# Performance work log

Measured on AMD Instinct MI355X. Metric: run time of the kernel, lower is better.

Reference implementation:

```python
import jax, jax.numpy as jnp
import numpy as np

N, E, IN_DIM, H, D, EDGE_DIM, T = 50000, 800000, 128, 4, 32, 32, 8
NEG_SLOPE = 0.2


def setup_inputs() -> dict:
    key = jax.random.key(0)
    ks = jax.random.split(key, 12)
    s = 0.1  # xavier-ish scale
    return {
        "h": jax.random.normal(ks[0], (N, IN_DIM), jnp.float32),
        "W": jax.random.normal(ks[1], (IN_DIM, D * H), jnp.float32) * s,
        "edge_emb": jax.random.normal(ks[2], (T, EDGE_DIM), jnp.float32) * s,
        "W_r": jax.random.normal(ks[3], (T, EDGE_DIM, EDGE_DIM * H), jnp.float32) * s,
        "a_l": jax.random.normal(ks[4], (1, H, D), jnp.float32) * s,
        "a_r": jax.random.normal(ks[5], (1, H, D), jnp.float32) * s,
        "a_e": jax.random.normal(ks[6], (1, H, EDGE_DIM), jnp.float32) * s,
        "res_w": jax.random.normal(ks[7], (IN_DIM, D * H), jnp.float32) * s,
        "res_b": jnp.zeros((D * H,), jnp.float32),
        "row": jax.random.randint(ks[8], (E,), 0, N),  # src node per edge
        "col": jax.random.randint(ks[9], (E,), 0, N),  # dst node per edge
        "etype": jax.random.randint(ks[10], (E,), 0, T),
    }


def reference(h, W, edge_emb, W_r, a_l, a_r, a_e, res_w, res_b, row, col, etype):
    # node projection: [N, H, D]
    emb = (h @ W).reshape(-1, H, D)

    # TypedLinear on edge-type embeddings. Since edge features depend only on
    # etype, compute the per-type result once, then gather per edge.
    e_t = jnp.einsum('te,tef->tf', edge_emb, W_r).reshape(T, H, EDGE_DIM)
    h_e_t = (a_e * e_t).sum(-1)            # [T, H]

    h_l = (a_l * emb).sum(-1)              # [N, H]
    h_r = (a_r * emb).sum(-1)              # [N, H]
    scores = h_l[row] + h_r[col] + h_e_t[etype]          # [E, H]
    scores = jax.nn.leaky_relu(scores, NEG_SLOPE)

    # segment softmax over edges sharing the same destination node (col)
    m = jax.ops.segment_max(scores, col, num_segments=N)  # [N, H]
    ex = jnp.exp(scores - m[col])
    denom = jax.ops.segment_sum(ex, col, num_segments=N)
    alpha = ex / denom[col]                # [E, H]

    # u_mul_e + scatter-sum to destination nodes
    msg = emb[row] * alpha[:, :, None]     # [E, H, D]
    agg = jax.ops.segment_sum(msg, col, num_segments=N)   # [N, H, D]

    # original permutes to [N, D, H] before flattening (d-major layout)
    out = jnp.transpose(agg, (0, 2, 1)).reshape(-1, D * H)
    out = out + h @ res_w + res_b          # residual
    return jax.nn.elu(out)
```

## Files before the change

kernel.cpp:

```cpp
#include <hip/hip_runtime.h>
#include <math.h>

#define NH 4
#define EDIM 32
#define NEG_SLOPE 0.2f
#define BSH 5
#define BCAP 1024

typedef __attribute__((ext_vector_type(8))) short short8;
typedef __attribute__((ext_vector_type(4))) float f32x4;
typedef __attribute__((ext_vector_type(2))) float f32x2;

__device__ __forceinline__ unsigned short f2bf(float f) {
    unsigned int x = __builtin_bit_cast(unsigned int, f);
    unsigned int r = (x + 0x7fffu + ((x >> 16) & 1u)) >> 16;
    return (unsigned short)r;
}
__device__ __forceinline__ float bf2f(unsigned short u) {
    unsigned int x = ((unsigned int)u) << 16;
    return __builtin_bit_cast(float, x);
}

__global__ __launch_bounds__(256) void k_prep(
    const float* __restrict__ W, const float* __restrict__ Rw,
    unsigned short* __restrict__ Wt, unsigned short* __restrict__ Rwt,
    int* __restrict__ bucket_cursor,
    const float* __restrict__ edge_emb, const float* __restrict__ W_r,
    const float* __restrict__ a_e, float* __restrict__ h_e_t)
{
    int tid = threadIdx.x;
    if (blockIdx.x < 64) {
        int idx = blockIdx.x * 256 + tid;
        int n = idx >> 7, k = idx & 127;
        Wt[n * 128 + k]  = f2bf(W[k * 128 + n]);
        Rwt[n * 128 + k] = f2bf(Rw[k * 128 + n]);
        if (idx < 2048) bucket_cursor[idx] = idx * BCAP;
    } else {
        int j = blockIdx.x - 64;
        int t = j >> 2;
        int ec = (j & 3) * 2 + (tid >> 7);
        int rem = tid & 127;
        float v = 0.f;
#pragma unroll
        for (int u = 0; u < 4; ++u) {
            int e = ec * 4 + u;
            v += edge_emb[t * EDIM + e] * W_r[(size_t)(t * EDIM + e) * 128 + rem];
        }
        v *= a_e[rem];
#pragma unroll
        for (int off = 16; off >= 1; off >>= 1)
            v += __shfl_xor(v, off);
        if ((rem & 31) == 0) atomicAdd(&h_e_t[t * NH + (rem >> 5)], v);
    }
}

__global__ __launch_bounds__(256) void k_gemm_fill(
    const float* __restrict__ A, const unsigned short* __restrict__ Wt,
    const unsigned short* __restrict__ Rwt, const float* __restrict__ Rb,
    const float* __restrict__ a_l, const float* __restrict__ a_r,
    unsigned short* __restrict__ EmbBf, unsigned short* __restrict__ ResBf,
    float* __restrict__ h_l, float* __restrict__ h_r, int M,
    const int* __restrict__ row, const int* __restrict__ col,
    const int* __restrict__ etype, int* __restrict__ bucket_cursor,
    unsigned* __restrict__ ebuf, int E, int NB, int nFill)
{
    __shared__ char lds[49152];
    int tid = threadIdx.x;

    if ((int)blockIdx.x < nFill) {
        int* bins = (int*)lds;
        int* base = bins + 2048;
        for (int i = tid; i < NB; i += 256) bins[i] = 0;
        __syncthreads();
        int lo = blockIdx.x * 4096;
        int ccol[16];
#pragma unroll
        for (int u = 0; u < 16; ++u) {
            int i = lo + tid + u * 256;
            int c = (i < E) ? col[i] : -1;
            ccol[u] = c;
            if (c >= 0) atomicAdd(&bins[c >> BSH], 1);
        }
        __syncthreads();
        for (int i = tid; i < NB; i += 256) {
            int c = bins[i];
            base[i] = c ? atomicAdd(&bucket_cursor[i], c) : 0;
            bins[i] = 0;
        }
        __syncthreads();
#pragma unroll
        for (int u = 0; u < 16; ++u) {
            int i = lo + tid + u * 256;
            int c = ccol[u];
            if (c >= 0) {
                int bk = c >> BSH;
                int p = base[bk] + atomicAdd(&bins[bk], 1);
                ebuf[p] = (unsigned)row[i] | ((unsigned)etype[i] << 16)
                        | ((unsigned)(c & 31) << 24);
            }
        }
        return;
    }

    int m0 = ((int)blockIdx.x - nFill) * 64;
#pragma unroll
    for (int i = 0; i < 4; ++i) {
        int c = tid + 256 * i;
        int r = c >> 4, kc = c & 15;
        int grow = m0 + r;
        float4 v0 = make_float4(0.f, 0.f, 0.f, 0.f), v1 = v0;
        if (grow < M) {
            v0 = *(const float4*)&A[(size_t)grow * 128 + kc * 8];
            v1 = *(const float4*)&A[(size_t)grow * 128 + kc * 8 + 4];
        }
        union { unsigned short u[8]; uint4 v; } p;
        p.u[0] = f2bf(v0.x); p.u[1] = f2bf(v0.y); p.u[2] = f2bf(v0.z); p.u[3] = f2bf(v0.w);
        p.u[4] = f2bf(v1.x); p.u[5] = f2bf(v1.y); p.u[6] = f2bf(v1.z); p.u[7] = f2bf(v1.w);
        int b = (r * 256 + kc * 16) ^ ((r & 7) << 4);
        *(uint4*)&lds[b] = p.v;
    }
#pragma unroll
    for (int i = 0; i < 8; ++i) {
        int c = tid + 256 * i;
        int n = c >> 4, kc = c & 15;
        uint4 v = *(const uint4*)&Wt[n * 128 + kc * 8];
        int b = 16384 + ((n * 256 + kc * 16) ^ ((n & 7) << 4));
        *(uint4*)&lds[b] = v;
    }
    __syncthreads();

    int w = tid >> 6, lane = tid & 63;
    int g = lane >> 4, l15 = lane & 15;
    int lrow = w * 16 + l15;

    short8 a[4];
#pragma unroll
    for (int s = 0; s < 4; ++s)
        a[s] = *(const short8*)&lds[(lrow * 256 + s * 64 + g * 16) ^ ((lrow & 7) << 4)];

    f32x4 acc[8];
#pragma unroll
    for (int f = 0; f < 8; ++f) acc[f] = (f32x4){0.f, 0.f, 0.f, 0.f};

#pragma unroll
    for (int f = 0; f < 8; ++f) {
        int n = f * 16 + l15;
        int nsw = (n & 7) << 4;
#pragma unroll
        for (int s = 0; s < 4; ++s) {
            short8 b = *(const short8*)&lds[16384 + ((n * 256 + s * 64 + g * 16) ^ nsw)];
            acc[f] = __builtin_amdgcn_mfma_f32_16x16x32_bf16(a[s], b, acc[f], 0, 0, 0);
        }
    }
#pragma unroll
    for (int f = 0; f < 8; ++f) {
        int col2 = f * 16 + l15;
#pragma unroll
        for (int reg = 0; reg < 4; ++reg) {
            int grow = m0 + w * 16 + g * 4 + reg;
            if (grow < M) EmbBf[(size_t)grow * 128 + col2] = f2bf(acc[f][reg]);
        }
    }
    {
        float alv[8], arv[8];
#pragma unroll
        for (int f = 0; f < 8; ++f) {
            alv[f] = a_l[f * 16 + l15];
            arv[f] = a_r[f * 16 + l15];
        }
#pragma unroll
        for (int reg = 0; reg < 4; ++reg) {
            float4 hl4, hr4;
#pragma unroll
            for (int hh = 0; hh < 4; ++hh) {
                float pl = alv[2 * hh] * acc[2 * hh][reg] + alv[2 * hh + 1] * acc[2 * hh + 1][reg];
                float pr = arv[2 * hh] * acc[2 * hh][reg] + arv[2 * hh + 1] * acc[2 * hh + 1][reg];
#pragma unroll
                for (int off = 8; off >= 1; off >>= 1) {
                    pl += __shfl_xor(pl, off);
                    pr += __shfl_xor(pr, off);
                }
                (&hl4.x)[hh] = pl;
                (&hr4.x)[hh] = pr;
            }
            int grow = m0 + w * 16 + g * 4 + reg;
            if (l15 == 0 && grow < M) {
                *(float4*)&h_l[(size_t)grow * 4] = hl4;
                *(float4*)&h_r[(size_t)grow * 4] = hr4;
            }
        }
    }

    __syncthreads();
#pragma unroll
    for (int i = 0; i < 8; ++i) {
        int c = tid + 256 * i;
        int n = c >> 4, kc = c & 15;
        uint4 v = *(const uint4*)&Rwt[n * 128 + kc * 8];
        int b = 16384 + ((n * 256 + kc * 16) ^ ((n & 7) << 4));
        *(uint4*)&lds[b] = v;
    }
    __syncthreads();

#pragma unroll
    for (int f = 0; f < 8; ++f) acc[f] = (f32x4){0.f, 0.f, 0.f, 0.f};
#pragma unroll
    for (int f = 0; f < 8; ++f) {
        int n = f * 16 + l15;
        int nsw = (n & 7) << 4;
#pragma unroll
        for (int s = 0; s < 4; ++s) {
            short8 b = *(const short8*)&lds[16384 + ((n * 256 + s * 64 + g * 16) ^ nsw)];
            acc[f] = __builtin_amdgcn_mfma_f32_16x16x32_bf16(a[s], b, acc[f], 0, 0, 0);
        }
    }
#pragma unroll
    for (int f = 0; f < 8; ++f) {
        int col2 = f * 16 + l15;
        float bias = Rb[col2];
#pragma unroll
        for (int reg = 0; reg < 4; ++reg) {
            int grow = m0 + w * 16 + g * 4 + reg;
            if (grow < M) ResBf[(size_t)grow * 128 + col2] = f2bf(acc[f][reg] + bias);
        }
    }
}

__global__ __launch_bounds__(256) void k_sort_aggregate(
    const unsigned* __restrict__ ebuf, const int* __restrict__ bucket_cursor,
    const float* __restrict__ h_l, const float* __restrict__ h_e_t,
    const float* __restrict__ h_r, const unsigned short* __restrict__ embBf,
    const unsigned short* __restrict__ resBf, float* __restrict__ out, int N)
{
    __shared__ int sedge[BCAP];
    __shared__ int cnt[32];
    __shared__ int scn[33];
    __shared__ char shalpha[4 * 1536];

    int b = blockIdx.x;
    int tid = threadIdx.x;
    int seg = b * BCAP;
    int m = bucket_cursor[b] - seg;

    if (tid < 32) cnt[tid] = 0;
    __syncthreads();
    for (int i = tid; i < m; i += 256)
        atomicAdd(&cnt[(ebuf[seg + i] >> 24) & 31], 1);
    __syncthreads();
    if (tid < 32) {
        int v = cnt[tid];
        int s = v;
#pragma unroll
        for (int off = 1; off < 32; off <<= 1) {
            int u2 = __shfl_up(s, off);
            if (tid >= off) s += u2;
        }
        scn[tid + 1] = s;
        if (tid == 0) scn[0] = 0;
        cnt[tid] = s - v;
    }
    __syncthreads();
    for (int i = tid; i < m; i += 256) {
        unsigned e = ebuf[seg + i];
        int p = atomicAdd(&cnt[(e >> 24) & 31], 1);
        sedge[p] = (int)(e & 0x00FFFFFFu);
    }
    __syncthreads();

    int w = tid >> 6, lane = tid & 63;
    int myh = lane >> 4;
    int l31 = lane & 31;
    int hq = l31 >> 3;
    int sel = lane >> 5;
    char* wb = &shalpha[w * 1536];
    const char* ab2 = wb + 256 + hq * 260;
    const char* embByte = (const char*)embBf;

    for (int it = 0; it < 8; ++it) {
        int nd = it * 4 + w;
        int n = b * 32 + nd;
        if (n >= N) break;
        int st0 = scn[nd];
        int deg = scn[nd + 1] - st0;
        float4 hrv = *(const float4*)&h_r[(size_t)n * 4];

        if (deg <= 64) {
            bool act = lane < deg;
            float p0 = 0.f, p1 = 0.f, p2 = 0.f, p3 = 0.f;
            if (act) {
                int pk = sedge[st0 + lane];
                int r = pk & 0xffff;
                float4 hl = *(const float4*)&h_l[(size_t)r * 4];
                float4 he = *(const float4*)&h_e_t[(size_t)(pk >> 16) * 4];
                float sc0 = hl.x + he.x + hrv.x; sc0 = sc0 > 0.f ? sc0 : NEG_SLOPE * sc0;
                float sc1 = hl.y + he.y + hrv.y; sc1 = sc1 > 0.f ? sc1 : NEG_SLOPE * sc1;
                float sc2 = hl.z + he.z + hrv.z; sc2 = sc2 > 0.f ? sc2 : NEG_SLOPE * sc2;
                float sc3 = hl.w + he.w + hrv.w; sc3 = sc3 > 0.f ? sc3 : NEG_SLOPE * sc3;
                p0 = __expf(sc0); p1 = __expf(sc1);
                p2 = __expf(sc2); p3 = __expf(sc3);
                *(int*)(wb + lane * 4) = (pk & 0xffff) << 8;
                *(float*)(wb + 256 + 0 * 260 + lane * 4) = p0;
                *(float*)(wb + 256 + 1 * 260 + lane * 4) = p1;
                *(float*)(wb + 256 + 2 * 260 + lane * 4) = p2;
                *(float*)(wb + 256 + 3 * 260 + lane * 4) = p3;
            }
            float d0 = p0, d1 = p1, d2 = p2, d3 = p3;
#pragma unroll
            for (int off = 32; off >= 1; off >>= 1) {
                d0 += __shfl_xor(d0, off); d1 += __shfl_xor(d1, off);
                d2 += __shfl_xor(d2, off); d3 += __shfl_xor(d3, off);
            }
            float den = hq == 0 ? d0 : hq == 1 ? d1 : hq == 2 ? d2 : d3;
            float inv = (deg > 0) ? __builtin_amdgcn_rcpf(den) : 0.f;

            f32x4 acc4 = (f32x4){0.f, 0.f, 0.f, 0.f};
            for (int q = 0; q < deg; q += 8) {
                unsigned ro[4]; float aq[4];
#pragma unroll
                for (int u = 0; u < 4; ++u) {
                    int qe = q + 2 * u + sel;
                    int qc = qe < deg ? qe : deg - 1;
                    ro[u] = *(const unsigned*)(wb + qc * 4);
                    float av = *(const float*)(ab2 + qc * 4);
                    aq[u] = (qe < deg) ? av : 0.f;
                }
                uint2 ev[4];
#pragma unroll
                for (int u = 0; u < 4; ++u)
                    ev[u] = *(const uint2*)(embByte + (size_t)(ro[u] + l31 * 8));
#pragma unroll
                for (int u = 0; u < 4; ++u) {
                    f32x4 ef;
                    ef.x = __builtin_bit_cast(float, ev[u].x << 16);
                    ef.y = __builtin_bit_cast(float, ev[u].x & 0xffff0000u);
                    ef.z = __builtin_bit_cast(float, ev[u].y << 16);
                    ef.w = __builtin_bit_cast(float, ev[u].y & 0xffff0000u);
                    acc4 = __builtin_elementwise_fma(
                        ef, (f32x4){aq[u], aq[u], aq[u], aq[u]}, acc4);
                }
            }
            acc4.x += __shfl_xor(acc4.x, 32);
            acc4.y += __shfl_xor(acc4.y, 32);
            acc4.z += __shfl_xor(acc4.z, 32);
            acc4.w += __shfl_xor(acc4.w, 32);

            if (lane < 32) {
                size_t ob = (size_t)n * 128;
                int bj = lane * 4;
                int h0 = bj >> 5;
#pragma unroll
                for (int u = 0; u < 4; ++u) {
                    int d = (bj + u) & 31;
                    float o = acc4[u] * inv + bf2f(resBf[ob + d * 4 + h0]);
                    out[ob + d * 4 + h0] = o > 0.f ? o : expm1f(o);
                }
            }
        } else {
            f32x2 acc2 = (f32x2){0.f, 0.f};
            float d0 = 0.f, d1 = 0.f, d2 = 0.f, d3 = 0.f;
            for (int base2 = 0; base2 < deg; base2 += 64) {
                int el = base2 + lane;
                if (el < deg) {
                    int pk = sedge[st0 + el];
                    float4 hl = *(const float4*)&h_l[(size_t)(pk & 0xffff) * 4];
                    float4 he = *(const float4*)&h_e_t[(size_t)(pk >> 16) * 4];
                    float sc0 = hl.x + he.x + hrv.x; sc0 = sc0 > 0.f ? sc0 : NEG_SLOPE * sc0;
                    float sc1 = hl.y + he.y + hrv.y; sc1 = sc1 > 0.f ? sc1 : NEG_SLOPE * sc1;
                    float sc2 = hl.z + he.z + hrv.z; sc2 = sc2 > 0.f ? sc2 : NEG_SLOPE * sc2;
                    float sc3 = hl.w + he.w + hrv.w; sc3 = sc3 > 0.f ? sc3 : NEG_SLOPE * sc3;
                    d0 += __expf(sc0); d1 += __expf(sc1);
                    d2 += __expf(sc2); d3 += __expf(sc3);
                }
            }
#pragma unroll
            for (int off = 32; off >= 1; off >>= 1) {
                d0 += __shfl_xor(d0, off); d1 += __shfl_xor(d1, off);
                d2 += __shfl_xor(d2, off); d3 += __shfl_xor(d3, off);
            }
            float den = myh == 0 ? d0 : myh == 1 ? d1 : myh == 2 ? d2 : d3;
            float inv = __builtin_amdgcn_rcpf(den);
            for (int base2 = 0; base2 < deg; base2 += 64) {
                int el = base2 + lane;
                float p0 = 0.f, p1 = 0.f, p2 = 0.f, p3 = 0.f;
                int r = 0;
                if (el < deg) {
                    int pk = sedge[st0 + el];
                    r = pk & 0xffff;
                    float4 hl = *(const float4*)&h_l[(size_t)r * 4];
                    float4 he = *(const float4*)&h_e_t[(size_t)(pk >> 16) * 4];
                    float sc0 = hl.x + he.x + hrv.x; sc0 = sc0 > 0.f ? sc0 : NEG_SLOPE * sc0;
                    float sc1 = hl.y + he.y + hrv.y; sc1 = sc1 > 0.f ? sc1 : NEG_SLOPE * sc1;
                    float sc2 = hl.z + he.z + hrv.z; sc2 = sc2 > 0.f ? sc2 : NEG_SLOPE * sc2;
                    float sc3 = hl.w + he.w + hrv.w; sc3 = sc3 > 0.f ? sc3 : NEG_SLOPE * sc3;
                    p0 = __expf(sc0); p1 = __expf(sc1);
                    p2 = __expf(sc2); p3 = __expf(sc3);
                }
                int cmax = (deg - base2 < 64) ? (deg - base2) : 64;
                for (int qq = 0; qq < cmax; ++qq) {
                    int rq = __shfl(r, qq);
                    float a0 = __shfl(p0, qq), a1 = __shfl(p1, qq);
                    float a2 = __shfl(p2, qq), a3 = __shfl(p3, qq);
                    float aqv = myh == 0 ? a0 : myh == 1 ? a1 : myh == 2 ? a2 : a3;
                    unsigned int ev = *(const unsigned int*)&embBf[(size_t)rq * 128 + lane * 2];
                    f32x2 ef;
                    ef.x = __builtin_bit_cast(float, ev << 16);
                    ef.y = __builtin_bit_cast(float, ev & 0xffff0000u);
                    acc2 = __builtin_elementwise_fma(ef, (f32x2){aqv, aqv}, acc2);
                }
            }
            int j0 = lane * 2;
            int h0 = j0 >> 5, dd0 = j0 & 31;
            size_t ob = (size_t)n * 128;
            float o0 = acc2.x * inv + bf2f(resBf[ob + dd0 * 4 + h0]);
            float o1 = acc2.y * inv + bf2f(resBf[ob + (dd0 + 1) * 4 + h0]);
            out[ob + dd0 * 4 + h0] = o0 > 0.f ? o0 : expm1f(o0);
            out[ob + (dd0 + 1) * 4 + h0] = o1 > 0.f ? o1 : expm1f(o1);
        }
    }
}

extern "C" void kernel_launch(void* const* d_in, const int* in_sizes, int n_in,
                              void* d_out, int out_size, void* d_ws, size_t ws_size,
                              hipStream_t stream)
{
    const float* h        = (const float*)d_in[0];
    const float* W        = (const float*)d_in[1];
    const float* edge_emb = (const float*)d_in[2];
    const float* W_r      = (const float*)d_in[3];
    const float* a_l      = (const float*)d_in[4];
    const float* a_r      = (const float*)d_in[5];
    const float* a_e      = (const float*)d_in[6];
    const float* res_w    = (const float*)d_in[7];
    const float* res_b    = (const float*)d_in[8];
    const int*   row      = (const int*)d_in[9];
    const int*   col      = (const int*)d_in[10];
    const int*   etype    = (const int*)d_in[11];
    float* out = (float*)d_out;

    int N = in_sizes[0] / 128;
    int E = in_sizes[9];
    int T = in_sizes[2] / EDIM;
    int NB = (N + 31) >> BSH;

    char* ws = (char*)d_ws;
    size_t off = 0;
    auto alloc = [&](size_t bytes) -> char* {
        char* p = ws + off;
        off = (off + bytes + 255) & ~(size_t)255;
        return p;
    };
    unsigned short* embBf = (unsigned short*)alloc((size_t)N * 128 * 2);
    unsigned short* resBf = (unsigned short*)alloc((size_t)N * 128 * 2);
    unsigned short* Wt    = (unsigned short*)alloc((size_t)128 * 128 * 2);
    unsigned short* Rwt   = (unsigned short*)alloc((size_t)128 * 128 * 2);
    float* h_l   = (float*)alloc((size_t)N * 4 * 4);
    float* h_r   = (float*)alloc((size_t)N * 4 * 4);
    float* h_e_t = (float*)alloc((size_t)T * 4 * 4);
    int* bucket_cursor = (int*)alloc(2048 * 4);
    unsigned* ebuf = (unsigned*)alloc((size_t)(NB + 1) * BCAP * 4);

    int nFill = (E + 4095) / 4096;
    int nGemm = (N + 63) / 64;

    hipMemsetAsync(h_e_t, 0, (size_t)T * NH * 4, stream);
    hipLaunchKernelGGL(k_prep, dim3(64 + T * 4), dim3(256), 0, stream,
                       W, res_w, Wt, Rwt, bucket_cursor,
                       edge_emb, W_r, a_e, h_e_t);
    hipLaunchKernelGGL(k_gemm_fill, dim3(nFill + nGemm), dim3(256), 0, stream,
                       h, Wt, Rwt, res_b, a_l, a_r, embBf, resBf, h_l, h_r, N,
                       row, col, etype, bucket_cursor, ebuf, E, NB, nFill);
    hipLaunchKernelGGL(k_sort_aggregate, dim3(NB), dim3(256), 0, stream,
                       ebuf, bucket_cursor, h_l, h_e_t, h_r, embBf, resBf, out, N);
}
```

Measured before the change: 94.22 us.

## Move edge bucketing fill into prep kernel and split GEMM into its own launch

Result: slower. 99.00 us (+5.1%).

```diff
diff --git a/kernel.cpp b/kernel.cpp
--- a/kernel.cpp
+++ b/kernel.cpp
@@ -21,22 +21,29 @@
     return __builtin_bit_cast(float, x);
 }
 
-__global__ __launch_bounds__(256) void k_prep(
+__global__ __launch_bounds__(256) void k_prep_fill(
     const float* __restrict__ W, const float* __restrict__ Rw,
     unsigned short* __restrict__ Wt, unsigned short* __restrict__ Rwt,
-    int* __restrict__ bucket_cursor,
     const float* __restrict__ edge_emb, const float* __restrict__ W_r,
-    const float* __restrict__ a_e, float* __restrict__ h_e_t)
+    const float* __restrict__ a_e, float* __restrict__ h_e_t,
+    const int* __restrict__ row, const int* __restrict__ col,
+    const int* __restrict__ etype, int* __restrict__ bucket_cursor,
+    unsigned* __restrict__ ebuf, int E, int NB, int T)
 {
+    __shared__ int bins[2048];
+    __shared__ int base[2048];
     int tid = threadIdx.x;
-    if (blockIdx.x < 64) {
-        int idx = blockIdx.x * 256 + tid;
+    int bid = blockIdx.x;
+
+    if (bid < 64) {
+        int idx = bid * 256 + tid;
         int n = idx >> 7, k = idx & 127;
         Wt[n * 128 + k]  = f2bf(W[k * 128 + n]);
         Rwt[n * 128 + k] = f2bf(Rw[k * 128 + n]);
-        if (idx < 2048) bucket_cursor[idx] = idx * BCAP;
-    } else {
-        int j = blockIdx.x - 64;
+        return;
+    }
+    if (bid < 64 + T * 4) {
+        int j = bid - 64;
         int t = j >> 2;
         int ec = (j & 3) * 2 + (tid >> 7);
         int rem = tid & 127;
@@ -51,58 +58,52 @@
         for (int off = 16; off >= 1; off >>= 1)
             v += __shfl_xor(v, off);
         if ((rem & 31) == 0) atomicAdd(&h_e_t[t * NH + (rem >> 5)], v);
-    }
-}
-
-__global__ __launch_bounds__(256) void k_gemm_fill(
+        return;
+    }
+
+    int fb = bid - 64 - T * 4;
+    for (int i = tid; i < NB; i += 256) bins[i] = 0;
+    __syncthreads();
+    int lo = fb * 4096;
+    int ccol[16];
+#pragma unroll
+    for (int u = 0; u < 16; ++u) {
+        int i = lo + tid + u * 256;
+        int c = (i < E) ? col[i] : -1;
+        ccol[u] = c;
+        if (c >= 0) atomicAdd(&bins[c >> BSH], 1);
+    }
+    __syncthreads();
+    for (int i = tid; i < NB; i += 256) {
+        int c = bins[i];
+        base[i] = c ? atomicAdd(&bucket_cursor[i], c) : 0;
+        bins[i] = 0;
+    }
+    __syncthreads();
+#pragma unroll
+    for (int u = 0; u < 16; ++u) {
+        int i = lo + tid + u * 256;
+        int c = ccol[u];
+        if (c >= 0) {
+            int bk = c >> BSH;
+            int p = bk * BCAP + base[bk] + atomicAdd(&bins[bk], 1);
+            ebuf[p] = (unsigned)row[i] | ((unsigned)etype[i] << 16)
+                    | ((unsigned)(c & 31) << 24);
+        }
+    }
+}
+
+__global__ __launch_bounds__(256) void k_gemm(
     const float* __restrict__ A, const unsigned short* __restrict__ Wt,
     const unsigned short* __restrict__ Rwt, const float* __restrict__ Rb,
     const float* __restrict__ a_l, const float* __restrict__ a_r,
     unsigned short* __restrict__ EmbBf, unsigned short* __restrict__ ResBf,
-    float* __restrict__ h_l, float* __restrict__ h_r, int M,
-    const int* __restrict__ row, const int* __restrict__ col,
-    const int* __restrict__ etype, int* __restrict__ bucket_cursor,
-    unsigned* __restrict__ ebuf, int E, int NB, int nFill)
+    float* __restrict__ h_l, float* __restrict__ h_r, int M)
 {
     __shared__ char lds[49152];
     int tid = threadIdx.x;
-
-    if ((int)blockIdx.x < nFill) {
-        int* bins = (int*)lds;
-        int* base = bins + 2048;
-        for (int i = tid; i < NB; i += 256) bins[i] = 0;
-        __syncthreads();
-        int lo = blockIdx.x * 4096;
-        int ccol[16];
-#pragma unroll
-        for (int u = 0; u < 16; ++u) {
-            int i = lo + tid + u * 256;
-            int c = (i < E) ? col[i] : -1;
-            ccol[u] = c;
-            if (c >= 0) atomicAdd(&bins[c >> BSH], 1);
-        }
-        __syncthreads();
-        for (int i = tid; i < NB; i += 256) {
-            int c = bins[i];
-            base[i] = c ? atomicAdd(&bucket_cursor[i], c) : 0;
-            bins[i] = 0;
-        }
-        __syncthreads();
-#pragma unroll
-        for (int u = 0; u < 16; ++u) {
-            int i = lo + tid + u * 256;
-            int c = ccol[u];
-            if (c >= 0) {
-                int bk = c >> BSH;
-                int p = base[bk] + atomicAdd(&bins[bk], 1);
-                ebuf[p] = (unsigned)row[i] | ((unsigned)etype[i] << 16)
-                        | ((unsigned)(c & 31) << 24);
-            }
-        }
-        return;
-    }
-
-    int m0 = ((int)blockIdx.x - nFill) * 64;
+    int m0 = blockIdx.x * 64;
+
 #pragma unroll
     for (int i = 0; i < 4; ++i) {
         int c = tid + 256 * i;
@@ -240,7 +241,7 @@
     int b = blockIdx.x;
     int tid = threadIdx.x;
     int seg = b * BCAP;
-    int m = bucket_cursor[b] - seg;
+    int m = bucket_cursor[b];
 
     if (tid < 32) cnt[tid] = 0;
     __syncthreads();
@@ -270,8 +271,9 @@
     int w = tid >> 6, lane = tid & 63;
     int myh = lane >> 4;
     int l31 = lane & 31;
+    int sel = lane >> 5;
     int hq = l31 >> 3;
-    int sel = lane >> 5;
+    int loff = l31 * 8;
     char* wb = &shalpha[w * 1536];
     const char* ab2 = wb + 256 + hq * 260;
     const char* embByte = (const char*)embBf;
@@ -287,10 +289,11 @@
         if (deg <= 64) {
             bool act = lane < deg;
             float p0 = 0.f, p1 = 0.f, p2 = 0.f, p3 = 0.f;
+            int roval = 0;
             if (act) {
                 int pk = sedge[st0 + lane];
-                int r = pk & 0xffff;
-                float4 hl = *(const float4*)&h_l[(size_t)r * 4];
+                roval = (pk & 0xffff) << 8;
+                float4 hl = *(const float4*)&h_l[(size_t)(pk & 0xffff) * 4];
                 float4 he = *(const float4*)&h_e_t[(size_t)(pk >> 16) * 4];
                 float sc0 = hl.x + he.x + hrv.x; sc0 = sc0 > 0.f ? sc0 : NEG_SLOPE * sc0;
                 float sc1 = hl.y + he.y + hrv.y; sc1 = sc1 > 0.f ? sc1 : NEG_SLOPE * sc1;
@@ -298,12 +301,13 @@
                 float sc3 = hl.w + he.w + hrv.w; sc3 = sc3 > 0.f ? sc3 : NEG_SLOPE * sc3;
                 p0 = __expf(sc0); p1 = __expf(sc1);
                 p2 = __expf(sc2); p3 = __expf(sc3);
-                *(int*)(wb + lane * 4) = (pk & 0xffff) << 8;
-                *(float*)(wb + 256 + 0 * 260 + lane * 4) = p0;
-                *(float*)(wb + 256 + 1 * 260 + lane * 4) = p1;
-                *(float*)(wb + 256 + 2 * 260 + lane * 4) = p2;
-                *(float*)(wb + 256 + 3 * 260 + lane * 4) = p3;
-            }
+            }
+            *(int*)(wb + lane * 4) = roval;
+            *(float*)(wb + 256 + 0 * 260 + lane * 4) = p0;
+            *(float*)(wb + 256 + 1 * 260 + lane * 4) = p1;
+            *(float*)(wb + 256 + 2 * 260 + lane * 4) = p2;
+            *(float*)(wb + 256 + 3 * 260 + lane * 4) = p3;
+
             float d0 = p0, d1 = p1, d2 = p2, d3 = p3;
 #pragma unroll
             for (int off = 32; off >= 1; off >>= 1) {
@@ -315,19 +319,17 @@
 
             f32x4 acc4 = (f32x4){0.f, 0.f, 0.f, 0.f};
             for (int q = 0; q < deg; q += 8) {
-                unsigned ro[4]; float aq[4];
+                int ro[4]; float aq[4];
 #pragma unroll
                 for (int u = 0; u < 4; ++u) {
                     int qe = q + 2 * u + sel;
-                    int qc = qe < deg ? qe : deg - 1;
-                    ro[u] = *(const unsigned*)(wb + qc * 4);
-                    float av = *(const float*)(ab2 + qc * 4);
-                    aq[u] = (qe < deg) ? av : 0.f;
+                    ro[u] = *(const int*)(wb + qe * 4);
+                    aq[u] = *(const float*)(ab2 + qe * 4);
                 }
                 uint2 ev[4];
 #pragma unroll
                 for (int u = 0; u < 4; ++u)
-                    ev[u] = *(const uint2*)(embByte + (size_t)(ro[u] + l31 * 8));
+                    ev[u] = *(const uint2*)(embByte + (size_t)(unsigned)(ro[u] + loff));
 #pragma unroll
                 for (int u = 0; u < 4; ++u) {
                     f32x4 ef;
@@ -343,18 +345,16 @@
             acc4.y += __shfl_xor(acc4.y, 32);
             acc4.z += __shfl_xor(acc4.z, 32);
             acc4.w += __shfl_xor(acc4.w, 32);
-
-            if (lane < 32) {
-                size_t ob = (size_t)n * 128;
-                int bj = lane * 4;
-                int h0 = bj >> 5;
-#pragma unroll
-                for (int u = 0; u < 4; ++u) {
-                    int d = (bj + u) & 31;
-                    float o = acc4[u] * inv + bf2f(resBf[ob + d * 4 + h0]);
-                    out[ob + d * 4 + h0] = o > 0.f ? o : expm1f(o);
-                }
-            }
+            float vlo = sel ? acc4.z : acc4.x;
+            float vhi = sel ? acc4.w : acc4.y;
+
+            int j0 = l31 * 4 + sel * 2;
+            int h0 = j0 >> 5, dd = j0 & 31;
+            size_t ob = (size_t)n * 128;
+            float o0 = vlo * inv + bf2f(resBf[ob + dd * 4 + h0]);
+            float o1 = vhi * inv + bf2f(resBf[ob + (dd + 1) * 4 + h0]);
+            out[ob + dd * 4 + h0] = o0 > 0.f ? o0 : expm1f(o0);
+            out[ob + (dd + 1) * 4 + h0] = o1 > 0.f ? o1 : expm1f(o1);
         } else {
             f32x2 acc2 = (f32x2){0.f, 0.f};
             float d0 = 0.f, d1 = 0.f, d2 = 0.f, d3 = 0.f;
@@ -455,20 +455,19 @@
     unsigned short* Rwt   = (unsigned short*)alloc((size_t)128 * 128 * 2);
     float* h_l   = (float*)alloc((size_t)N * 4 * 4);
     float* h_r   = (float*)alloc((size_t)N * 4 * 4);
-    float* h_e_t = (float*)alloc((size_t)T * 4 * 4);
     int* bucket_cursor = (int*)alloc(2048 * 4);
+    float* h_e_t = (float*)alloc((size_t)T * NH * 4);
     unsigned* ebuf = (unsigned*)alloc((size_t)(NB + 1) * BCAP * 4);
 
     int nFill = (E + 4095) / 4096;
     int nGemm = (N + 63) / 64;
 
-    hipMemsetAsync(h_e_t, 0, (size_t)T * NH * 4, stream);
-    hipLaunchKernelGGL(k_prep, dim3(64 + T * 4), dim3(256), 0, stream,
-                       W, res_w, Wt, Rwt, bucket_cursor,
-                       edge_emb, W_r, a_e, h_e_t);
-    hipLaunchKernelGGL(k_gemm_fill, dim3(nFill + nGemm), dim3(256), 0, stream,
-                       h, Wt, Rwt, res_b, a_l, a_r, embBf, resBf, h_l, h_r, N,
-                       row, col, etype, bucket_cursor, ebuf, E, NB, nFill);
+    hipMemsetAsync(bucket_cursor, 0, 8192 + (size_t)T * NH * 4, stream);
+    hipLaunchKernelGGL(k_prep_fill, dim3(64 + T * 4 + nFill), dim3(256), 0, stream,
+                       W, res_w, Wt, Rwt, edge_emb, W_r, a_e, h_e_t,
+                       row, col, etype, bucket_cursor, ebuf, E, NB, T);
+    hipLaunchKernelGGL(k_gemm, dim3(nGemm), dim3(256), 0, stream,
+                       h, Wt, Rwt, res_b, a_l, a_r, embBf, resBf, h_l, h_r, N);
     hipLaunchKernelGGL(k_sort_aggregate, dim3(NB), dim3(256), 0, stream,
                        ebuf, bucket_cursor, h_l, h_e_t, h_r, embBf, resBf, out, N);
 }
```
